# Kernel optimization log

Measured on AMD Instinct MI355X. Metric: run time of the kernel, lower is better.

The kernel has to match this reference:

```python
import jax, jax.numpy as jnp
import numpy as np
from jax import lax

B, C, L, O, H, W = 256, 768, 64, 768, 9, 9
C2, C3 = 2 * C // 3, C // 3  # convh_2 / convl_1 output channels


def _c1x1(x, w, b):
    # 1x1 conv, w: (out,in), x: (b,in,h,w)
    return jnp.einsum('oc,bchw->bohw', w, x) + b[None, :, None, None]


def _conv3x3(x, w, b=None):
    out = lax.conv_general_dilated(x, w, (1, 1), 'SAME', dimension_numbers=('NCHW', 'OIHW', 'NCHW'))
    if b is not None:
        out = out + b[None, :, None, None]
    return out


def _cossim(a, b):
    # torch F.cosine_similarity over dim=1, eps=1e-8
    num = jnp.sum(a * b, axis=1)
    den = jnp.maximum(jnp.linalg.norm(a, axis=1) * jnp.linalg.norm(b, axis=1), 1e-8)
    return num / den


def _ufilt1d(x, size, axis):
    # scipy.ndimage.uniform_filter1d, mode='reflect' (== numpy 'symmetric')
    r = size // 2
    pad = [(r, r) if a == axis else (0, 0) for a in range(x.ndim)]
    xp = jnp.moveaxis(jnp.pad(x, pad, mode='symmetric'), axis, -1)
    c = jnp.cumsum(xp, axis=-1)
    c = jnp.concatenate([jnp.zeros_like(c[..., :1]), c], axis=-1)
    out = (c[..., size:] - c[..., :-size]) / size
    return jnp.moveaxis(out, -1, axis)


def _ufilt(x, size):
    # skimage ssim with channel_axis=1 on a (b,c,h,w) array treats (b,h,w) as
    # the 3 spatial dims (batch included!) and loops over channels.
    for ax in (0, 2, 3):
        x = _ufilt1d(x, size, ax)
    return x


def _ssim_map(x, y, win=7):
    NP = win ** 3  # 3 spatial dims (b,h,w)
    cov_norm = NP / (NP - 1.0)
    c1, c2 = 0.01 ** 2, 0.03 ** 2  # data_range = 1.0
    ux, uy = _ufilt(x, win), _ufilt(y, win)
    vx = cov_norm * (_ufilt(x * x, win) - ux * ux)
    vy = cov_norm * (_ufilt(y * y, win) - uy * uy)
    vxy = cov_norm * (_ufilt(x * y, win) - ux * uy)
    return ((2 * ux * uy + c1) * (2 * vxy + c2)) / ((ux * ux + uy * uy + c1) * (vx + vy + c2))


def setup_inputs() -> dict:
    key = jax.random.key(0)
    ks = jax.random.split(key, 40)
    n = lambda i, shape, s=1.0: jax.random.normal(ks[i], shape, jnp.float32) * s
    return {
        'x': n(0, (B, C, H, W)),
        'y': n(1, (B, L, H, W)),
        'w_convh1': n(2, (C, C), C ** -0.5), 'b_convh1': n(3, (C,), 0.01),
        'w_conv1_1': n(4, (C, C), C ** -0.5), 'b_conv1_1': n(5, (C,), 0.01),
        'w_convh2': n(6, (C2, C), C ** -0.5), 'b_convh2': n(7, (C2,), 0.01),
        'w_convl1': n(8, (C3, L), L ** -0.5), 'b_convl1': n(9, (C3,), 0.01),
        'w_convh3': n(10, (1, C), C ** -0.5), 'b_convh3': n(11, (1,), 0.01),
        'w_convl2': n(12, (1, L), L ** -0.5), 'b_convl2': n(13, (1,), 0.01),
        'w_conv1_2': n(14, (2, 2), 0.7), 'b_conv1_2': n(15, (2,), 0.01),
        'w_convl3': n(16, (2, L), L ** -0.5), 'b_convl3': n(17, (2,), 0.01),
        'w_cc1': n(18, (1, 2), 0.7), 'b_cc1': n(19, (1,), 0.01),
        'w_pool': n(20, (2, 1, 3, 3), 1.0 / 3.0), 'b_pool': n(21, (2,), 0.01),
        'w_fc1': n(22, (324, 324), 324 ** -0.5), 'b_fc1': n(23, (324,), 0.01),
        'w_fc2': n(24, (81, 324), 324 ** -0.5), 'b_fc2': n(25, (81,), 0.01),
        'w_bconv': n(26, (O, C, 3, 3), (C * 9) ** -0.5),
        'bn_gamma': 1.0 + n(27, (O,), 0.1), 'bn_beta': n(28, (O,), 0.1),
        'bn_mean': n(29, (O,), 0.1),
        'bn_var': 1.0 + 0.1 * jax.random.uniform(ks[30], (O,), jnp.float32),
    }


def reference(x, y, w_convh1, b_convh1, w_conv1_1, b_conv1_1, w_convh2, b_convh2,
              w_convl1, b_convl1, w_convh3, b_convh3, w_convl2, b_convl2,
              w_conv1_2, b_conv1_2, w_convl3, b_convl3, w_cc1, b_cc1,
              w_pool, b_pool, w_fc1, b_fc1, w_fc2, b_fc2,
              w_bconv, bn_gamma, bn_beta, bn_mean, bn_var):
    b = x.shape[0]
    fuse_1 = _c1x1(x, w_convh1, b_convh1)                                   # (b,C,9,9)
    fuse_2 = _c1x1(jnp.concatenate([_c1x1(x, w_convh2, b_convh2),
                                    _c1x1(y, w_convl1, b_convl1)], axis=1),
                   w_conv1_1, b_conv1_1)                                     # (b,C,9,9)
    fuse_3 = _c1x1(jnp.concatenate([_c1x1(x, w_convh3, b_convh3),
                                    _c1x1(y, w_convl2, b_convl2)], axis=1),
                   w_conv1_2, b_conv1_2)                                     # (b,2,9,9)
    fuse_4 = _c1x1(y, w_convl3, b_convl3)                                    # (b,2,9,9)
    cor_1 = _cossim(fuse_1, fuse_2)[:, None]                                 # (b,1,9,9)
    ssim_value = lax.stop_gradient(_ssim_map(fuse_3, fuse_4))                # detach() in torch
    fuse2_1 = fuse_1 + 0.5 * (1.0 - cor_1) * fuse_2
    fuse2_2 = _c1x1(fuse_4 + ssim_value * fuse_3, w_cc1, b_cc1)              # (b,1,9,9)
    cor2_1 = _cossim(fuse2_1, jnp.broadcast_to(fuse2_2, fuse2_1.shape))[:, None]
    fuse3_1 = fuse2_1 + 0.5 * (1.0 - cor2_1 + _c1x1(ssim_value, w_cc1, b_cc1)) * fuse2_2
    # fuse2_2 has 1 channel -> channel mean == channel max == fuse2_2
    xc = jnp.concatenate([fuse2_2, _conv3x3(fuse2_2, w_pool, b_pool), fuse2_2], axis=1)  # (b,4,9,9)
    xc = xc.reshape(b, -1)
    h1 = jax.nn.gelu(xc @ w_fc1.T + b_fc1, approximate=False)
    xweight = jax.nn.leaky_relu(h1 @ w_fc2.T + b_fc2, 0.01).reshape(b, 1, H, W)
    xout = xweight * fuse3_1 + fuse3_1
    xout = _conv3x3(xout, w_bconv)
    scale = (bn_gamma / jnp.sqrt(bn_var + 1e-5))[None, :, None, None]
    xout = (xout - bn_mean[None, :, None, None]) * scale + bn_beta[None, :, None, None]
    return jax.nn.leaky_relu(xout, 0.01)
```

## Files before the change

kernel.cpp:

```cpp
#include <hip/hip_runtime.h>
#include <hip/hip_bf16.h>
#include <math.h>

#define BATCH 256
#define CCH 768
#define LCH 64
#define PP 81
#define CHW 3072

typedef __attribute__((ext_vector_type(8))) short short8v;
typedef __attribute__((ext_vector_type(4))) float f32x4;

#define GLL16(gp, lp) __builtin_amdgcn_global_load_lds( \
    (const __attribute__((address_space(1))) void*)(gp), \
    (__attribute__((address_space(3))) void*)(lp), 16, 0, 0)

__global__ __launch_bounds__(256) void kw_compose(
    const float* __restrict__ W11, const float* __restrict__ Wh2,
    const float* __restrict__ Wl1, const float* __restrict__ bh2,
    const float* __restrict__ bl1, const float* __restrict__ b11,
    const float* __restrict__ Wh1,
    __hip_bfloat16* __restrict__ WAp, __hip_bfloat16* __restrict__ WBp,
    __hip_bfloat16* __restrict__ Wh1p, float* __restrict__ beff)
{
    int o = blockIdx.x;
    int t = threadIdx.x;
    int ot = o >> 4, l15o = o & 15;
    const float* w11row = W11 + (size_t)o * CCH;
    for (int c = t; c < CCH; c += 256) {
        float s = 0.f;
        for (int k = 0; k < 512; ++k) s = fmaf(w11row[k], Wh2[(size_t)k*CCH + c], s);
        int ch = c >> 5, kg = (c >> 3) & 3, j = c & 7;
        size_t idx = (((size_t)ot*24 + ch) << 9) + (size_t)(kg*16 + l15o)*8 + j;
        WAp[idx]  = __float2bfloat16(s);
        Wh1p[idx] = __float2bfloat16(Wh1[(size_t)o*CCH + c]);
    }
    if (t < LCH) {
        float s = 0.f;
        for (int k = 0; k < 256; ++k) s = fmaf(w11row[512+k], Wl1[k*LCH + t], s);
        int ch = t >> 5, kg = (t >> 3) & 3, j = t & 7;
        size_t idx = (((size_t)ot*2 + ch) << 9) + (size_t)(kg*16 + l15o)*8 + j;
        WBp[idx] = __float2bfloat16(s);
    }
    if (t == 0) {
        float s = b11[o];
        for (int k = 0; k < 512; ++k) s = fmaf(w11row[k], bh2[k], s);
        for (int k = 0; k < 256; ++k) s = fmaf(w11row[512+k], bl1[k], s);
        beff[o] = s;
    }
}

__global__ __launch_bounds__(256) void k_wprep(
    const float* __restrict__ Wb, __hip_bfloat16* __restrict__ Wp)
{
    int ot = blockIdx.x;
    int i  = blockIdx.y*256 + threadIdx.x;
    int oi = i / 96, c8 = i - oi*96;
    const float* src = Wb + ((size_t)(ot*16 + oi)*CCH + c8*8)*9;
    int ch = c8 >> 2;
    int lane8 = (((c8 & 3)*16) + oi)*8;
    #pragma unroll
    for (int t = 0; t < 9; ++t) {
        short8v v;
        #pragma unroll
        for (int j = 0; j < 8; ++j) {
            __hip_bfloat16 h = __float2bfloat16(src[j*9 + t]);
            v[j] = __builtin_bit_cast(short, h);
        }
        *(short8v*)(Wp + ((((size_t)(t*48 + ot))*24 + ch) << 9) + lane8) = v;
    }
}

__global__ __launch_bounds__(256) void k_fcprep(
    const float* __restrict__ Wfc1, const float* __restrict__ Wfc2,
    float* __restrict__ T1, float* __restrict__ T2)
{
    int n = blockIdx.x*256 + threadIdx.x;
    if (n < 324*324) { int i = n / 324, j = n - i*324; T1[(size_t)j*324 + i] = Wfc1[n]; }
    if (n < 81*324)  { int q = n / 324, j = n - q*324; T2[(size_t)j*81 + q]  = Wfc2[n]; }
}

__global__ __launch_bounds__(256) void k_xprep_f34(
    const float* __restrict__ x, const float* __restrict__ y,
    const float* __restrict__ wh3, const float* __restrict__ bh3,
    const float* __restrict__ wl2, const float* __restrict__ bl2,
    const float* __restrict__ W12, const float* __restrict__ b12,
    const float* __restrict__ Wl3, const float* __restrict__ bl3,
    __hip_bfloat16* __restrict__ xT2, __hip_bfloat16* __restrict__ yT2,
    float* __restrict__ f3, float* __restrict__ f4, float* __restrict__ Af)
{
    int b = blockIdx.x;
    int tid = threadIdx.x;
    __shared__ float ls[64][82];
    __shared__ float red[243][4];
    __shared__ float zz[10][81];
    __shared__ float tb[10][81];
    int q = tid / 81, p81 = tid - q*81;
    bool act = tid < 243;
    for (int i = tid; i < 24*32; i += 256) {
        int ch = i >> 5, c = i & 31;
        xT2[(((size_t)b*24 + ch)*96 + 81)*32 + c] = __float2bfloat16(0.f);
    }
    if (tid < 2*32) {
        int ch = tid >> 5, c = tid & 31;
        yT2[(((size_t)b*2 + ch)*96 + 81)*32 + c] = __float2bfloat16(0.f);
    }
    float sx = 0.f;
    for (int c0 = 0; c0 < CCH; c0 += 64) {
        int ch0 = c0 >> 5;
        __syncthreads();
        for (int i = tid; i < 64*81; i += 256) {
            int c = i / 81, p = i - c*81;
            ls[c][p] = x[((size_t)b*CCH + c0 + c)*PP + p];
        }
        __syncthreads();
        for (int i = tid; i < 81*64; i += 256) {
            int p = i >> 6, c = i & 63;
            int ch = ch0 + (c >> 5), cc = c & 31;
            int s = cc >> 3, j = cc & 7;
            int slot = s ^ ((p >> 1) & 3);
            xT2[(((size_t)b*24 + ch)*96 + p)*32 + slot*8 + j] = __float2bfloat16(ls[c][p]);
        }
        if (act)
            for (int c = q; c < 64; c += 3)
                sx = fmaf(wh3[c0+c], ls[c][p81], sx);
    }
    __syncthreads();
    for (int i = tid; i < 64*81; i += 256) {
        int c = i / 81, p = i - c*81;
        ls[c][p] = y[((size_t)b*LCH + c)*PP + p];
    }
    __syncthreads();
    for (int i = tid; i < 81*64; i += 256) {
        int p = i >> 6, c = i & 63;
        int ch = c >> 5, cc = c & 31;
        int s = cc >> 3, j = cc & 7;
        int slot = s ^ ((p >> 1) & 3);
        yT2[(((size_t)b*2 + ch)*96 + p)*32 + slot*8 + j] = __float2bfloat16(ls[c][p]);
    }
    float sy = 0.f, s40 = 0.f, s41 = 0.f;
    if (act) {
        for (int c = q; c < 64; c += 3) {
            float v = ls[c][p81];
            sy  = fmaf(wl2[c], v, sy);
            s40 = fmaf(Wl3[c], v, s40);
            s41 = fmaf(Wl3[LCH+c], v, s41);
        }
        red[tid][0]=sx; red[tid][1]=sy; red[tid][2]=s40; red[tid][3]=s41;
    }
    __syncthreads();
    if (tid < 81) {
        float SX  = red[tid][0]+red[tid+81][0]+red[tid+162][0];
        float SY  = red[tid][1]+red[tid+81][1]+red[tid+162][1];
        float S40 = red[tid][2]+red[tid+81][2]+red[tid+162][2];
        float S41 = red[tid][3]+red[tid+81][3]+red[tid+162][3];
        float t3a = SX + bh3[0];
        float t3b = SY + bl2[0];
        float f30 = W12[0]*t3a + W12[1]*t3b + b12[0];
        float f31 = W12[2]*t3a + W12[3]*t3b + b12[1];
        float f40 = S40 + bl3[0];
        float f41 = S41 + bl3[1];
        f3[(b*2+0)*PP+tid] = f30; f3[(b*2+1)*PP+tid] = f31;
        f4[(b*2+0)*PP+tid] = f40; f4[(b*2+1)*PP+tid] = f41;
        zz[0][tid]=f30; zz[1][tid]=f40; zz[2][tid]=f30*f30; zz[3][tid]=f40*f40; zz[4][tid]=f30*f40;
        zz[5][tid]=f31; zz[6][tid]=f41; zz[7][tid]=f31*f31; zz[8][tid]=f41*f41; zz[9][tid]=f31*f41;
    }
    __syncthreads();
    for (int i = tid; i < 10*81; i += 256) {
        int f = i / 81, p = i - f*81;
        int yy = p/9, xx = p - yy*9;
        float s = 0.f;
        #pragma unroll
        for (int d = -3; d <= 3; ++d) {
            int j = xx + d;
            j = (j < 0) ? (-1-j) : ((j > 8) ? (17-j) : j);
            s += zz[f][yy*9+j];
        }
        tb[f][p] = s * (1.f/7.f);
    }
    __syncthreads();
    for (int i = tid; i < 10*81; i += 256) {
        int f = i / 81, p = i - f*81;
        int yy = p/9, xx = p - yy*9;
        float s = 0.f;
        #pragma unroll
        for (int d = -3; d <= 3; ++d) {
            int j = yy + d;
            j = (j < 0) ? (-1-j) : ((j > 8) ? (17-j) : j);
            s += tb[f][j*9+xx];
        }
        Af[((size_t)b*10 + f)*81 + p] = s * (1.f/7.f);
    }
}

__global__ __launch_bounds__(256) void k_ssim_b2(
    const float* __restrict__ A, float* __restrict__ U)
{
    int col0 = blockIdx.x * 32;
    int tid = threadIdx.x;
    __shared__ float lsb[256][33];
    for (int i = tid; i < 256*32; i += 256) {
        int j = i >> 5, cc = i & 31;
        int col = col0 + cc;
        lsb[j][cc] = (col < 810) ? A[(size_t)j*810 + col] : 0.f;
    }
    __syncthreads();
    for (int i = tid; i < 256*32; i += 256) {
        int b = i >> 5, cc = i & 31;
        float s = 0.f;
        #pragma unroll
        for (int d = -3; d <= 3; ++d) {
            int j = b + d;
            j = (j < 0) ? (-1-j) : ((j > 255) ? (511-j) : j);
            s += lsb[j][cc];
        }
        int col = col0 + cc;
        if (col < 810) U[(size_t)b*810 + col] = s * (1.f/7.f);
    }
}

__global__ __launch_bounds__(128) void k_fc(
    const float* __restrict__ U, const float* __restrict__ f3,
    const float* __restrict__ f4, const float* __restrict__ wcc,
    const float* __restrict__ bcc,
    const float* __restrict__ wpool, const float* __restrict__ bpool,
    const float* __restrict__ T1, const float* __restrict__ bfc1,
    const float* __restrict__ T2, const float* __restrict__ bfc2,
    float* __restrict__ f22, float* __restrict__ ccs,
    float* __restrict__ xw)
{
    int b = blockIdx.x;
    int tid = threadIdx.x;
    __shared__ float xc[324];
    __shared__ float h1[324];
    __shared__ float pr[2][81], ps[2][81];
    const float cov = 343.f/342.f, C1c = 1e-4f, C2c = 9e-4f;
    for (int i = tid; i < 162; i += 128) {
        int k = i / 81, p = i - k*81;
        const float* u = U + (size_t)b*810 + (k*5)*81 + p;
        float ux = u[0], uy = u[81], uxx = u[162], uyy = u[243], uxy = u[324];
        float vx = cov*(uxx - ux*ux), vy = cov*(uyy - uy*uy), vxy = cov*(uxy - ux*uy);
        float S = ((2.f*ux*uy + C1c)*(2.f*vxy + C2c)) /
                  ((ux*ux + uy*uy + C1c)*(vx + vy + C2c));
        float a = f4[(b*2+k)*81+p] + S*f3[(b*2+k)*81+p];
        pr[k][p] = wcc[k]*a;
        ps[k][p] = wcc[k]*S;
    }
    __syncthreads();
    if (tid < 81) {
        float fv = pr[0][tid] + pr[1][tid] + bcc[0];
        float cv = ps[0][tid] + ps[1][tid] + bcc[0];
        f22[b*81+tid] = fv;
        ccs[b*81+tid] = cv;
        xc[tid] = fv; xc[243+tid] = fv;
    }
    __syncthreads();
    for (int i = tid; i < 162; i += 128) {
        int k = i / 81, p = i - k*81;
        int yy = p/9, xx = p - yy*9;
        float s = bpool[k];
        #pragma unroll
        for (int dy = -1; dy <= 1; ++dy)
            #pragma unroll
            for (int dx = -1; dx <= 1; ++dx) {
                int Y = yy+dy, X = xx+dx;
                if (Y >= 0 && Y < 9 && X >= 0 && X < 9)
                    s = fmaf(wpool[k*9 + (dy+1)*3 + (dx+1)], xc[Y*9+X], s);
            }
        xc[81+i] = s;
    }
    __syncthreads();
    for (int i = tid; i < 324; i += 128) {
        float s = bfc1[i];
        for (int j = 0; j < 324; ++j) s = fmaf(T1[(size_t)j*324 + i], xc[j], s);
        h1[i] = 0.5f*s*(1.f + erff(s*0.70710678118654752f));
    }
    __syncthreads();
    for (int qq = tid; qq < 81; qq += 128) {
        float s = bfc2[qq];
        for (int j = 0; j < 324; ++j) s = fmaf(T2[(size_t)j*81 + qq], h1[j], s);
        xw[b*81+qq] = (s > 0.f) ? s : 0.01f*s;
    }
}

__global__ __launch_bounds__(256, 3) void k_fuse12_mfma(
    const __hip_bfloat16* __restrict__ xT2,
    const __hip_bfloat16* __restrict__ yT2,
    const __hip_bfloat16* __restrict__ Wh1p,
    const __hip_bfloat16* __restrict__ WAp,
    const __hip_bfloat16* __restrict__ WBp,
    const float* __restrict__ bh1, const float* __restrict__ beff,
    __hip_bfloat16* __restrict__ f1, __hip_bfloat16* __restrict__ f2)
{
    int oy = blockIdx.x;
    int b  = blockIdx.y;
    int tid = threadIdx.x;
    int w    = tid >> 6;
    int g    = w >> 1;
    int nh   = w & 1;
    int lane = tid & 63;
    int l15  = lane & 15;
    int kg   = lane >> 4;

    __shared__ __align__(16) __hip_bfloat16 ls[6*CHW];

    int spoff[3];
    #pragma unroll
    for (int nl = 0; nl < 3; ++nl) {
        int p = (nh*3 + nl)*16 + l15;
        int sp = (p < PP) ? p : 81;
        spoff[nl] = sp*32 + ((kg ^ ((sp >> 1) & 3)) << 3);
    }

    f32x4 acc[6][3];
    #pragma unroll
    for (int m = 0; m < 6; ++m)
        #pragma unroll
        for (int nl = 0; nl < 3; ++nl)
            acc[m][nl] = (f32x4){0.f,0.f,0.f,0.f};

    const __hip_bfloat16* xb = xT2 + (size_t)b*24*CHW;
    const __hip_bfloat16* yb = yT2 + (size_t)b*2*CHW;
    const __hip_bfloat16* Wsel = g ? WAp : Wh1p;
    int otb = oy*6;

    for (int grp = 0; grp < 4; ++grp) {
        __syncthreads();
        const __hip_bfloat16* src = xb + (size_t)grp*6*CHW;
        #pragma unroll
        for (int k = 0; k < 9; ++k) {
            int it = w + 4*k;
            GLL16(src + it*512 + lane*8, &ls[it*512]);
        }
        __syncthreads();
        for (int cc = 0; cc < 6; ++cc) {
            int ch = grp*6 + cc;
            const __hip_bfloat16* lb = &ls[cc*CHW];
            short8v a[6];
            #pragma unroll
            for (int m = 0; m < 6; ++m)
                a[m] = *(const short8v*)(Wsel + ((((size_t)(otb + m))*24 + ch) << 9) + (lane<<3));
            #pragma unroll
            for (int nl = 0; nl < 3; ++nl) {
                short8v bf = *(const short8v*)&lb[spoff[nl]];
                #pragma unroll
                for (int m = 0; m < 6; ++m)
                    acc[m][nl] = __builtin_amdgcn_mfma_f32_16x16x32_bf16(a[m], bf, acc[m][nl], 0, 0, 0);
            }
        }
    }

    __syncthreads();
    #pragma unroll
    for (int k = 0; k < 3; ++k) {
        int it = w + 4*k;
        GLL16(yb + it*512 + lane*8, &ls[it*512]);
    }
    __syncthreads();
    if (g == 1) {
        for (int ch2 = 0; ch2 < 2; ++ch2) {
            const __hip_bfloat16* lb = &ls[ch2*CHW];
            short8v a[6];
            #pragma unroll
            for (int m = 0; m < 6; ++m)
                a[m] = *(const short8v*)(WBp + ((((size_t)(otb + m))*2 + ch2) << 9) + (lane<<3));
            #pragma unroll
            for (int nl = 0; nl < 3; ++nl) {
                short8v bf = *(const short8v*)&lb[spoff[nl]];
                #pragma unroll
                for (int m = 0; m < 6; ++m)
                    acc[m][nl] = __builtin_amdgcn_mfma_f32_16x16x32_bf16(a[m], bf, acc[m][nl], 0, 0, 0);
            }
        }
    }

    __hip_bfloat16* dst = g ? f2 : f1;
    const float* bias = g ? beff : bh1;
    #pragma unroll
    for (int m = 0; m < 6; ++m) {
        #pragma unroll
        for (int r = 0; r < 4; ++r) {
            int o = (otb + m)*16 + kg*4 + r;
            float bb = bias[o];
            #pragma unroll
            for (int nl = 0; nl < 3; ++nl) {
                int p = (nh*3 + nl)*16 + l15;
                if (p < PP)
                    dst[((size_t)b*CCH + o)*PP + p] = __float2bfloat16(acc[m][nl][r] + bb);
            }
        }
    }
}

__global__ __launch_bounds__(256) void k_finalize(
    const __hip_bfloat16* __restrict__ f1, const __hip_bfloat16* __restrict__ f2,
    const float* __restrict__ f22, const float* __restrict__ ccs,
    const float* __restrict__ xw,
    __hip_bfloat16* __restrict__ inb2)
{
    int b = blockIdx.x;
    int tid = threadIdx.x;
    __shared__ float red[243][5];
    __shared__ float sal[81], sga[81], scm[81];
    __shared__ float ls[64][82];
    for (int i = tid; i < 24*32; i += 256) {
        int ch = i >> 5, c = i & 31;
        inb2[(((size_t)b*24 + ch)*96 + 81)*32 + c] = __float2bfloat16(0.f);
    }
    bool act = tid < 243;
    float Sxx=0.f, Syy=0.f, Sxy=0.f, Sx=0.f, Sy=0.f;
    const __hip_bfloat16* A = f1 + (size_t)b*CCH*PP;
    const __hip_bfloat16* C = f2 + (size_t)b*CCH*PP;
    if (act) {
        for (int c0 = 0; c0 < CCH; c0 += 3) {
            float u = __bfloat162float(A[(size_t)c0*PP + tid]);
            float v = __bfloat162float(C[(size_t)c0*PP + tid]);
            Sxx = fmaf(u,u,Sxx); Syy = fmaf(v,v,Syy); Sxy = fmaf(u,v,Sxy);
            Sx += u; Sy += v;
        }
        red[tid][0]=Sxx; red[tid][1]=Syy; red[tid][2]=Sxy; red[tid][3]=Sx; red[tid][4]=Sy;
    }
    __syncthreads();
    if (tid < 81) {
        float xx = red[tid][0]+red[tid+81][0]+red[tid+162][0];
        float yy = red[tid][1]+red[tid+81][1]+red[tid+162][1];
        float xy = red[tid][2]+red[tid+81][2]+red[tid+162][2];
        float sx = red[tid][3]+red[tid+81][3]+red[tid+162][3];
        float sy = red[tid][4]+red[tid+81][4]+red[tid+162][4];
        float cor1 = xy / fmaxf(sqrtf(xx)*sqrtf(yy), 1e-8f);
        float al = 0.5f*(1.f - cor1);
        float sum21 = sx + al*sy;
        float n21 = sqrtf(fmaxf(xx + 2.f*al*xy + al*al*yy, 0.f));
        int t = b*81 + tid;
        float fv = f22[t];
        float cor2 = (fv * sum21) / fmaxf(n21 * 27.712812921102035f * fabsf(fv), 1e-8f);
        float be = 0.5f*(1.f - cor2 + ccs[t]);
        sal[tid] = al;
        sga[tid] = be * fv;
        scm[tid] = 1.f + xw[t];
    }
    for (int c0 = 0; c0 < CCH; c0 += 64) {
        int ch0 = c0 >> 5;
        __syncthreads();
        for (int i = tid; i < 64*81; i += 256) {
            int c = i / 81, p = i - c*81;
            size_t gidx = ((size_t)b*CCH + c0 + c)*PP + p;
            float u = __bfloat162float(f1[gidx]);
            float v = __bfloat162float(f2[gidx]);
            ls[c][p] = scm[p]*(u + sal[p]*v + sga[p]);
        }
        __syncthreads();
        for (int i = tid; i < 81*64; i += 256) {
            int p = i >> 6, c = i & 63;
            int ch = ch0 + (c >> 5), cc = c & 31;
            int s = cc >> 3, j = cc & 7;
            int slot = s ^ ((p >> 1) & 3);
            inb2[(((size_t)b*24 + ch)*96 + p)*32 + slot*8 + j] = __float2bfloat16(ls[c][p]);
        }
    }
}

__global__ __launch_bounds__(256, 2) void k_bconv_mfma(
    const __hip_bfloat16* __restrict__ inb2,
    const __hip_bfloat16* __restrict__ Wp,
    const float* __restrict__ bn_g, const float* __restrict__ bn_b,
    const float* __restrict__ bn_m, const float* __restrict__ bn_v,
    float* __restrict__ out)
{
    int oy = blockIdx.x;
    int b0 = blockIdx.y * 2;
    int tid = threadIdx.x;
    int w    = tid >> 6;
    int bi   = w >> 1;
    int nh   = w & 1;
    int lane = tid & 63;
    int l15  = lane & 15;
    int kg   = lane >> 4;

    __shared__ __align__(16) __hip_bfloat16 ls[6*CHW];

    int spoff[9][3];
    #pragma unroll
    for (int t = 0; t < 9; ++t) {
        int dy = t/3 - 1, dx = t%3 - 1;
        #pragma unroll
        for (int nl = 0; nl < 3; ++nl) {
            int p = (nh*3 + nl)*16 + l15;
            int yy = p/9, xx = p - yy*9;
            int Y = yy + dy, X = xx + dx;
            bool ok = (p < PP) && (Y >= 0) && (Y < 9) && (X >= 0) && (X < 9);
            int sp = ok ? (Y*9 + X) : 81;
            spoff[t][nl] = sp*32 + ((kg ^ ((sp >> 1) & 3)) << 3);
        }
    }

    f32x4 acc[6][3];
    #pragma unroll
    for (int m = 0; m < 6; ++m)
        #pragma unroll
        for (int nl = 0; nl < 3; ++nl)
            acc[m][nl] = (f32x4){0.f,0.f,0.f,0.f};

    const __hip_bfloat16* img0 = inb2 + (size_t)(b0    )*24*CHW;
    const __hip_bfloat16* img1 = inb2 + (size_t)(b0 + 1)*24*CHW;
    int otb = oy*6;

    for (int grp = 0; grp < 8; ++grp) {
        __syncthreads();
        #pragma unroll
        for (int k = 0; k < 9; ++k) {
            int it = w + 4*k;
            int bb = it / 18;
            int r  = it - bb*18;
            int cc = r / 6, sub = r - cc*6;
            const __hip_bfloat16* src =
                (bb ? img1 : img0) + (size_t)(grp*3 + cc)*CHW + sub*512;
            GLL16(src + lane*8, &ls[(size_t)(bb*3 + cc)*CHW + sub*512]);
        }
        __syncthreads();
        for (int cc = 0; cc < 3; ++cc) {
            int ch = grp*3 + cc;
            const __hip_bfloat16* lb = &ls[(size_t)(bi*3 + cc)*CHW];
            #pragma unroll
            for (int t = 0; t < 9; ++t) {
                short8v a[6];
                #pragma unroll
                for (int m = 0; m < 6; ++m)
                    a[m] = *(const short8v*)(Wp + (((size_t)(t*48 + otb + m)*24 + ch) << 9) + (lane<<3));
                #pragma unroll
                for (int nl = 0; nl < 3; ++nl) {
                    short8v bf = *(const short8v*)&lb[spoff[t][nl]];
                    #pragma unroll
                    for (int m = 0; m < 6; ++m)
                        acc[m][nl] = __builtin_amdgcn_mfma_f32_16x16x32_bf16(a[m], bf, acc[m][nl], 0, 0, 0);
                }
            }
        }
    }

    int b = b0 + bi;
    #pragma unroll
    for (int m = 0; m < 6; ++m) {
        #pragma unroll
        for (int r = 0; r < 4; ++r) {
            int o = (otb + m)*16 + kg*4 + r;
            float sc = bn_g[o] * rsqrtf(bn_v[o] + 1e-5f);
            float mn = bn_m[o], bt = bn_b[o];
            #pragma unroll
            for (int nl = 0; nl < 3; ++nl) {
                int p = (nh*3 + nl)*16 + l15;
                if (p < PP) {
                    float v = (acc[m][nl][r] - mn) * sc + bt;
                    out[((size_t)b*CCH + o)*PP + p] = (v > 0.f) ? v : 0.01f*v;
                }
            }
        }
    }
}

extern "C" void kernel_launch(void* const* d_in, const int* in_sizes, int n_in,
                              void* d_out, int out_size, void* d_ws, size_t ws_size,
                              hipStream_t stream)
{
    (void)in_sizes; (void)n_in; (void)out_size; (void)ws_size;
    const float* x    = (const float*)d_in[0];
    const float* y    = (const float*)d_in[1];
    const float* Wh1  = (const float*)d_in[2];
    const float* bh1  = (const float*)d_in[3];
    const float* W11  = (const float*)d_in[4];
    const float* b11  = (const float*)d_in[5];
    const float* Wh2  = (const float*)d_in[6];
    const float* bh2  = (const float*)d_in[7];
    const float* Wl1  = (const float*)d_in[8];
    const float* bl1  = (const float*)d_in[9];
    const float* wh3  = (const float*)d_in[10];
    const float* bh3  = (const float*)d_in[11];
    const float* wl2  = (const float*)d_in[12];
    const float* bl2  = (const float*)d_in[13];
    const float* W12  = (const float*)d_in[14];
    const float* b12  = (const float*)d_in[15];
    const float* Wl3  = (const float*)d_in[16];
    const float* bl3  = (const float*)d_in[17];
    const float* wcc  = (const float*)d_in[18];
    const float* bcc  = (const float*)d_in[19];
    const float* wpool= (const float*)d_in[20];
    const float* bpool= (const float*)d_in[21];
    const float* Wfc1 = (const float*)d_in[22];
    const float* bfc1 = (const float*)d_in[23];
    const float* Wfc2 = (const float*)d_in[24];
    const float* bfc2 = (const float*)d_in[25];
    const float* Wb   = (const float*)d_in[26];
    const float* bng  = (const float*)d_in[27];
    const float* bnb  = (const float*)d_in[28];
    const float* bnm  = (const float*)d_in[29];
    const float* bnv  = (const float*)d_in[30];
    float* out = (float*)d_out;
    float* ws = (float*)d_ws;

    size_t off = 0;
    float* beff  = ws + off; off += CCH;
    float* f3    = ws + off; off += BATCH*2*PP;
    float* f4    = ws + off; off += BATCH*2*PP;
    float* Af    = ws + off; off += BATCH*10*PP;
    float* Uf    = ws + off; off += BATCH*10*PP;
    float* f22   = ws + off; off += BATCH*PP;
    float* ccs   = ws + off; off += BATCH*PP;
    float* xw    = ws + off; off += BATCH*PP;
    float* T1    = ws + off; off += 324*324;
    float* T2    = ws + off; off += 324*81;
    off = (off + 3) & ~(size_t)3;
    __hip_bfloat16* Wh1p = (__hip_bfloat16*)(ws + off); off += (size_t)48*24*512/2;
    __hip_bfloat16* WAp  = (__hip_bfloat16*)(ws + off); off += (size_t)48*24*512/2;
    __hip_bfloat16* WBp  = (__hip_bfloat16*)(ws + off); off += (size_t)48*2*512/2;
    __hip_bfloat16* yT2  = (__hip_bfloat16*)(ws + off); off += (size_t)BATCH*2*CHW/2;
    __hip_bfloat16* f1b  = (__hip_bfloat16*)(ws + off); off += (size_t)BATCH*CCH*PP/2;
    __hip_bfloat16* f2b  = (__hip_bfloat16*)(ws + off); off += (size_t)BATCH*CCH*PP/2;
    off = (off + 3) & ~(size_t)3;
    __hip_bfloat16* inb2 = (__hip_bfloat16*)(ws + off); off += (size_t)BATCH*24*CHW/2;
    __hip_bfloat16* Wp   = (__hip_bfloat16*)(ws + off); off += (size_t)9*48*24*512/2;
    __hip_bfloat16* xT2 = inb2;

    kw_compose<<<dim3(CCH), dim3(256), 0, stream>>>(W11, Wh2, Wl1, bh2, bl1, b11, Wh1, WAp, WBp, Wh1p, beff);
    k_wprep<<<dim3(48, 6), dim3(256), 0, stream>>>(Wb, Wp);
    k_fcprep<<<dim3(411), dim3(256), 0, stream>>>(Wfc1, Wfc2, T1, T2);
    k_xprep_f34<<<dim3(BATCH), dim3(256), 0, stream>>>(x, y, wh3, bh3, wl2, bl2, W12, b12, Wl3, bl3, xT2, yT2, f3, f4, Af);
    k_ssim_b2<<<dim3(26), dim3(256), 0, stream>>>(Af, Uf);
    k_fc<<<dim3(BATCH), dim3(128), 0, stream>>>(Uf, f3, f4, wcc, bcc, wpool, bpool, T1, bfc1, T2, bfc2, f22, ccs, xw);
    k_fuse12_mfma<<<dim3(8, BATCH), dim3(256), 0, stream>>>(xT2, yT2, Wh1p, WAp, WBp, bh1, beff, f1b, f2b);
    k_finalize<<<dim3(BATCH), dim3(256), 0, stream>>>(f1b, f2b, f22, ccs, xw, inb2);
    k_bconv_mfma<<<dim3(8, BATCH/2), dim3(256), 0, stream>>>(inb2, Wp, bng, bnb, bnm, bnv, out);
}
```

Before: 697.6 us.

## Process two batches per fuse12 block with 512 threads and raise occupancy bounds

The fuse12 MFMA kernel now handles two batch elements per block using 8 waves. Each pair of waves shares the weight tile loads, so weight reads per batch are amortised. The channel groups in shared memory are cut from 6 to 3 per batch so the LDS footprint stays the same. The launch bounds of fuse12 and bconv are raised to ask for more resident waves, which risks register spills with an acc array of 18 f32x4 values.

```diff
diff --git a/kernel.cpp b/kernel.cpp
--- a/kernel.cpp
+++ b/kernel.cpp
@@ -283,7 +283,7 @@
     }
 }
 
-__global__ __launch_bounds__(256, 3) void k_fuse12_mfma(
+__global__ __launch_bounds__(512, 4) void k_fuse12_mfma(
     const __hip_bfloat16* __restrict__ xT2,
     const __hip_bfloat16* __restrict__ yT2,
     const __hip_bfloat16* __restrict__ Wh1p,
@@ -293,10 +293,11 @@
     __hip_bfloat16* __restrict__ f1, __hip_bfloat16* __restrict__ f2)
 {
     int oy = blockIdx.x;
-    int b  = blockIdx.y;
+    int b0 = blockIdx.y * 2;
     int tid = threadIdx.x;
     int w    = tid >> 6;
-    int g    = w >> 1;
+    int bi   = w >> 2;
+    int g    = (w >> 1) & 1;
     int nh   = w & 1;
     int lane = tid & 63;
     int l15  = lane & 15;
@@ -319,23 +320,31 @@
         for (int nl = 0; nl < 3; ++nl)
             acc[m][nl] = (f32x4){0.f,0.f,0.f,0.f};
 
-    const __hip_bfloat16* xb = xT2 + (size_t)b*24*CHW;
-    const __hip_bfloat16* yb = yT2 + (size_t)b*2*CHW;
+    const __hip_bfloat16* xb0 = xT2 + (size_t)(b0    )*24*CHW;
+    const __hip_bfloat16* xb1 = xT2 + (size_t)(b0 + 1)*24*CHW;
+    const __hip_bfloat16* yb0 = yT2 + (size_t)(b0    )*2*CHW;
+    const __hip_bfloat16* yb1 = yT2 + (size_t)(b0 + 1)*2*CHW;
     const __hip_bfloat16* Wsel = g ? WAp : Wh1p;
     int otb = oy*6;
 
-    for (int grp = 0; grp < 4; ++grp) {
-        __syncthreads();
-        const __hip_bfloat16* src = xb + (size_t)grp*6*CHW;
-        #pragma unroll
-        for (int k = 0; k < 9; ++k) {
-            int it = w + 4*k;
-            GLL16(src + it*512 + lane*8, &ls[it*512]);
-        }
-        __syncthreads();
-        for (int cc = 0; cc < 6; ++cc) {
-            int ch = grp*6 + cc;
-            const __hip_bfloat16* lb = &ls[cc*CHW];
+    for (int grp = 0; grp < 8; ++grp) {
+        __syncthreads();
+        #pragma unroll
+        for (int k = 0; k < 5; ++k) {
+            int it = w + 8*k;
+            if (it < 36) {
+                int bb = it / 18;
+                int r  = it - bb*18;
+                int cc = r / 6, sub = r - cc*6;
+                const __hip_bfloat16* src =
+                    (bb ? xb1 : xb0) + (size_t)(grp*3 + cc)*CHW + sub*512;
+                GLL16(src + lane*8, &ls[(size_t)(bb*3 + cc)*CHW + sub*512]);
+            }
+        }
+        __syncthreads();
+        for (int cc = 0; cc < 3; ++cc) {
+            int ch = grp*3 + cc;
+            const __hip_bfloat16* lb = &ls[(size_t)(bi*3 + cc)*CHW];
             short8v a[6];
             #pragma unroll
             for (int m = 0; m < 6; ++m)
@@ -353,13 +362,17 @@
     __syncthreads();
     #pragma unroll
     for (int k = 0; k < 3; ++k) {
-        int it = w + 4*k;
-        GLL16(yb + it*512 + lane*8, &ls[it*512]);
+        int it = w + 8*k;
+        int bb = it / 12;
+        int r  = it - bb*12;
+        int cc2 = r / 6, sub = r - cc2*6;
+        const __hip_bfloat16* src = (bb ? yb1 : yb0) + (size_t)cc2*CHW + sub*512;
+        GLL16(src + lane*8, &ls[(size_t)(bb*2 + cc2)*CHW + sub*512]);
     }
     __syncthreads();
     if (g == 1) {
         for (int ch2 = 0; ch2 < 2; ++ch2) {
-            const __hip_bfloat16* lb = &ls[ch2*CHW];
+            const __hip_bfloat16* lb = &ls[(size_t)(bi*2 + ch2)*CHW];
             short8v a[6];
             #pragma unroll
             for (int m = 0; m < 6; ++m)
@@ -374,6 +387,7 @@
         }
     }
 
+    int b = b0 + bi;
     __hip_bfloat16* dst = g ? f2 : f1;
     const float* bias = g ? beff : bh1;
     #pragma unroll
@@ -460,7 +474,7 @@
     }
 }
 
-__global__ __launch_bounds__(256, 2) void k_bconv_mfma(
+__global__ __launch_bounds__(256, 4) void k_bconv_mfma(
     const __hip_bfloat16* __restrict__ inb2,
     const __hip_bfloat16* __restrict__ Wp,
     const float* __restrict__ bn_g, const float* __restrict__ bn_b,
@@ -626,7 +640,7 @@
     k_xprep_f34<<<dim3(BATCH), dim3(256), 0, stream>>>(x, y, wh3, bh3, wl2, bl2, W12, b12, Wl3, bl3, xT2, yT2, f3, f4, Af);
     k_ssim_b2<<<dim3(26), dim3(256), 0, stream>>>(Af, Uf);
     k_fc<<<dim3(BATCH), dim3(128), 0, stream>>>(Uf, f3, f4, wcc, bcc, wpool, bpool, T1, bfc1, T2, bfc2, f22, ccs, xw);
-    k_fuse12_mfma<<<dim3(8, BATCH), dim3(256), 0, stream>>>(xT2, yT2, Wh1p, WAp, WBp, bh1, beff, f1b, f2b);
+    k_fuse12_mfma<<<dim3(8, BATCH/2), dim3(512), 0, stream>>>(xT2, yT2, Wh1p, WAp, WBp, bh1, beff, f1b, f2b);
     k_finalize<<<dim3(BATCH), dim3(256), 0, stream>>>(f1b, f2b, f22, ccs, xw, inb2);
     k_bconv_mfma<<<dim3(8, BATCH/2), dim3(256), 0, stream>>>(inb2, Wp, bng, bnb, bnm, bnv, out);
 }
```

After: 1.381 ms. 98.0% more time.
